# Kernel tuning notes

Hardware: AMD Instinct MI355X
Metric: run time of the kernel (lower is better)

Reference implementation:

```python
import jax, jax.numpy as jnp
import numpy as np

N = 100000
E = 1600000
D_IN = 64
D_OUT = 64
NUM_GRAPHS = 64
EPS = 1e-5


def setup_inputs() -> dict:
    key = jax.random.key(0)
    ks = jax.random.split(key, 8)
    x = jax.random.normal(ks[0], (N, D_IN), dtype=jnp.float32)
    edge_index = jax.random.randint(ks[1], (2, E), 0, N, dtype=jnp.int64)
    edge_attr = jax.random.uniform(ks[2], (E,), dtype=jnp.float32)
    batch_index = jnp.sort(jax.random.randint(ks[3], (N,), 0, NUM_GRAPHS, dtype=jnp.int64))
    s = 1.0 / np.sqrt(D_IN)
    W_rel = jax.random.uniform(ks[4], (D_OUT, D_IN), minval=-s, maxval=s, dtype=jnp.float32)
    b_rel = jax.random.uniform(ks[5], (D_OUT,), minval=-s, maxval=s, dtype=jnp.float32)
    W_root = jax.random.uniform(ks[6], (D_OUT, D_IN), minval=-s, maxval=s, dtype=jnp.float32)
    gn_weight = jnp.ones((D_OUT,), dtype=jnp.float32)
    gn_bias = jnp.zeros((D_OUT,), dtype=jnp.float32)
    gn_mean_scale = jnp.ones((D_OUT,), dtype=jnp.float32)
    return {"x": x, "edge_index": edge_index, "edge_attr": edge_attr,
            "batch_index": batch_index, "W_rel": W_rel, "b_rel": b_rel,
            "W_root": W_root, "gn_weight": gn_weight, "gn_bias": gn_bias,
            "gn_mean_scale": gn_mean_scale}


def reference(x, edge_index, edge_attr, batch_index, W_rel, b_rel, W_root,
              gn_weight, gn_bias, gn_mean_scale):
    src, dst = edge_index[0], edge_index[1]
    # GraphConv: out = W_rel @ sum_{j in N(i)} e_ij * x_j + W_root @ x_i + b
    msg = edge_attr[:, None] * x[src]                      # [E, D_IN]
    agg = jax.ops.segment_sum(msg, dst, num_segments=N)    # [N, D_IN]
    h = agg @ W_rel.T + b_rel + x @ W_root.T               # [N, D_OUT]
    h = jax.nn.relu(h)
    # GraphNorm over per-graph segments
    cnt = jax.ops.segment_sum(jnp.ones((N, 1), h.dtype), batch_index,
                              num_segments=NUM_GRAPHS)      # [G, 1]
    mean = jax.ops.segment_sum(h, batch_index, num_segments=NUM_GRAPHS) / cnt
    out = h - mean[batch_index] * gn_mean_scale
    var = jax.ops.segment_sum(out * out, batch_index, num_segments=NUM_GRAPHS) / cnt
    std = jnp.sqrt(var + EPS)[batch_index]
    return gn_weight * out / std + gn_bias
```

## Files before the change

kernel.cpp:

```cpp
#include <hip/hip_runtime.h>

#define N_NODES 100000
#define N_EDGES 1600000
#define D 64
#define NUM_GRAPHS 64
#define EPS 1e-5f

#define BSHIFT 9
#define NPB 512
#define NBUCKETS ((N_NODES + NPB - 1) / NPB)
#define BCAP 12288
#define A_THREADS 1024
#define A_EPT 8
#define A_CHUNK (A_THREADS * A_EPT)
#define NBLK_A ((N_EDGES + A_CHUNK - 1) / A_CHUNK)
#define XB ((N_NODES * 64 / 8 + 255) / 256)

#define SCAN_T 256
#define SCAN_E 8
#define SCAN_CHUNK (SCAN_T * SCAN_E)
#define NSCAN ((N_NODES + SCAN_CHUNK - 1) / SCAN_CHUNK)

typedef float f32x4 __attribute__((ext_vector_type(4)));
typedef short bf16x8 __attribute__((ext_vector_type(8)));

__device__ __forceinline__ ushort f32_to_bf16_rne(float v) {
    unsigned int bits = __float_as_uint(v);
    return (ushort)((bits + 0x7FFFu + ((bits >> 16) & 1u)) >> 16);
}

__global__ __launch_bounds__(256) void xcast_init_kernel(
    const float* __restrict__ x, ushort* __restrict__ xh,
    int* __restrict__ bucket_cur, float* __restrict__ gsum,
    float* __restrict__ gsum2, float* __restrict__ gcnt)
{
    if (blockIdx.x < XB) {
        int i = blockIdx.x * blockDim.x + threadIdx.x;
        if (i >= N_NODES * 64 / 8) return;
        const float4* src = reinterpret_cast<const float4*>(x) + (size_t)i * 2;
        float4 v0 = src[0], v1 = src[1];
        float vf[8] = {v0.x, v0.y, v0.z, v0.w, v1.x, v1.y, v1.z, v1.w};
        union { ushort us[8]; uint4 u4; } o;
        #pragma unroll
        for (int j = 0; j < 8; ++j) o.us[j] = f32_to_bf16_rne(vf[j]);
        reinterpret_cast<uint4*>(xh)[i] = o.u4;
    } else {
        int i = (blockIdx.x - XB) * 256 + threadIdx.x;
        if (i < 256) bucket_cur[i] = i * BCAP;
        if (i < NUM_GRAPHS * 64) { gsum[i] = 0.f; gsum2[i] = 0.f; }
        if (i < 64) gcnt[i] = 0.f;
    }
}

__global__ __launch_bounds__(A_THREADS) void binA_kernel(
    const int* __restrict__ src_idx, const int* __restrict__ dst_idx,
    const float* __restrict__ ea, int* __restrict__ bucket_cursor,
    unsigned long long* __restrict__ binned)
{
    __shared__ int hist[NBUCKETS];
    __shared__ int lbase[NBUCKETS];
    int tid = threadIdx.x;
    if (tid < NBUCKETS) hist[tid] = 0;
    __syncthreads();

    int base = blockIdx.x * A_CHUNK;
    int srcv[A_EPT], dstv[A_EPT];
    float wv[A_EPT];
    #pragma unroll
    for (int i = 0; i < A_EPT; ++i) {
        int e = base + i * A_THREADS + tid;
        if (e < N_EDGES) {
            srcv[i] = src_idx[e];
            dstv[i] = dst_idx[e];
            wv[i]   = ea[e];
            atomicAdd(&hist[dstv[i] >> BSHIFT], 1);
        } else {
            dstv[i] = -1; srcv[i] = 0; wv[i] = 0.f;
        }
    }
    __syncthreads();
    if (tid < NBUCKETS) lbase[tid] = atomicAdd(&bucket_cursor[tid], hist[tid]);
    __syncthreads();
    if (tid < NBUCKETS) hist[tid] = 0;
    __syncthreads();
    #pragma unroll
    for (int i = 0; i < A_EPT; ++i) {
        if (dstv[i] >= 0) {
            int b = dstv[i] >> BSHIFT;
            int r = atomicAdd(&hist[b], 1);
            unsigned int lo = (unsigned int)(srcv[i] | ((dstv[i] & (NPB - 1)) << 17));
            unsigned long long pv = (unsigned long long)lo |
                ((unsigned long long)__float_as_uint(wv[i]) << 32);
            binned[lbase[b] + r] = pv;
        }
    }
}

__global__ __launch_bounds__(256) void binB_kernel(
    const unsigned long long* __restrict__ binned,
    const int* __restrict__ bucket_cur,
    int2* __restrict__ offsets2, unsigned int* __restrict__ csr)
{
    __shared__ int dcnt[NPB];
    __shared__ int doff[NPB];
    __shared__ int psum[256];
    int tid = threadIdx.x;
    int b = blockIdx.x;
    int beg = b * BCAP;
    int n = bucket_cur[b] - beg;

    for (int i = tid; i < NPB; i += 256) dcnt[i] = 0;
    __syncthreads();
    for (int j = tid; j < n; j += 256) {
        unsigned long long pv = binned[beg + j];
        atomicAdd(&dcnt[((unsigned int)pv) >> 17], 1);
    }
    __syncthreads();
    int e0 = dcnt[2 * tid], e1 = dcnt[2 * tid + 1];
    psum[tid] = e0 + e1;
    __syncthreads();
    for (int off = 1; off < 256; off <<= 1) {
        int v = psum[tid];
        int a = (tid >= off) ? psum[tid - off] : 0;
        __syncthreads();
        psum[tid] = v + a;
        __syncthreads();
    }
    int ex = (tid == 0) ? 0 : psum[tid - 1];
    doff[2 * tid] = ex;
    doff[2 * tid + 1] = ex + e0;
    __syncthreads();
    for (int i = tid; i < NPB; i += 256) {
        int node = (b << BSHIFT) + i;
        if (node < N_NODES) {
            int s = beg + doff[i];
            int e = beg + ((i + 1 < NPB) ? doff[i + 1] : n);
            offsets2[node] = make_int2(s, e);
        }
        dcnt[i] = doff[i];
    }
    __syncthreads();
    for (int j = tid; j < n; j += 256) {
        unsigned long long pv = binned[beg + j];
        unsigned int lo = (unsigned int)pv;
        unsigned int wbits = (unsigned int)(pv >> 32);
        int dlo = lo >> 17;
        int r = atomicAdd(&dcnt[dlo], 1);
        unsigned int field = ((wbits + 0x7FFFu + ((wbits >> 16) & 1u)) >> 16) & 0x7FFFu;
        csr[beg + r] = (lo & 0x1FFFFu) | (field << 17);
    }
}

__global__ __launch_bounds__(256) void gatherh_kernel(
    const ushort* __restrict__ xh, const int2* __restrict__ offsets2,
    const unsigned int* __restrict__ csr, ushort* __restrict__ agg)
{
    int wid = (int)((blockIdx.x * blockDim.x + threadIdx.x) >> 6);
    if (wid >= N_NODES) return;
    int lane = threadIdx.x & 63;
    int2 o2 = offsets2[wid];
    int beg = __builtin_amdgcn_readfirstlane(o2.x);
    int end = __builtin_amdgcn_readfirstlane(o2.y);
    float acc[8];
    #pragma unroll
    for (int u = 0; u < 8; ++u) acc[u] = 0.f;
    int j = beg;
    for (; j + 7 < end; j += 8) {
        unsigned int e[8];
        #pragma unroll
        for (int u = 0; u < 8; ++u) e[u] = csr[j + u];
        float xv[8];
        #pragma unroll
        for (int u = 0; u < 8; ++u)
            xv[u] = __uint_as_float((unsigned int)xh[(size_t)(e[u] & 0x1FFFFu) * 64 + lane] << 16);
        #pragma unroll
        for (int u = 0; u < 8; ++u)
            acc[u] = fmaf(__uint_as_float((e[u] >> 17) << 16), xv[u], acc[u]);
    }
    for (; j < end; ++j) {
        unsigned int e0 = csr[j];
        float xv = __uint_as_float((unsigned int)xh[(size_t)(e0 & 0x1FFFFu) * 64 + lane] << 16);
        acc[0] = fmaf(__uint_as_float((e0 >> 17) << 16), xv, acc[0]);
    }
    float a = ((acc[0] + acc[1]) + (acc[2] + acc[3])) +
              ((acc[4] + acc[5]) + (acc[6] + acc[7]));
    agg[(size_t)wid * 64 + lane] = f32_to_bf16_rne(a);
}

#define DB 128
__global__ __launch_bounds__(256) void dense_mfma16_kernel(
    const ushort* __restrict__ agg, const ushort* __restrict__ xh,
    ushort* __restrict__ hout,
    const float* __restrict__ W_rel, const float* __restrict__ b_rel,
    const float* __restrict__ W_root)
{
    __shared__ unsigned int Bf[4][4][64][4];
    int tid = threadIdx.x;

    #pragma unroll
    for (int g = 0; g < 8; ++g) {
        int q = tid * 8 + g;
        int i4   = (q & 1) * 4;
        int lane = (q >> 1) & 63;
        int dt   = (q >> 7) & 3;
        int kt   = (q >> 9) & 3;
        int d = dt * 16 + (lane & 15);
        int k = kt * 32 + (lane >> 4) * 8 + i4;
        const float* Wsrc = (k < 64) ? (W_rel + d * 64 + k)
                                     : (W_root + d * 64 + (k - 64));
        float4 w = *reinterpret_cast<const float4*>(Wsrc);
        unsigned int b0 = f32_to_bf16_rne(w.x);
        unsigned int b1 = f32_to_bf16_rne(w.y);
        unsigned int b2 = f32_to_bf16_rne(w.z);
        unsigned int b3 = f32_to_bf16_rne(w.w);
        int u = i4 >> 1;
        Bf[kt][dt][lane][u]     = b0 | (b1 << 16);
        Bf[kt][dt][lane][u + 1] = b2 | (b3 << 16);
    }
    __syncthreads();

    int wid = tid >> 6, lane = tid & 63;
    int nbase = blockIdx.x * DB + wid * 32;
    int r = lane & 15;
    int k0 = (lane >> 4) * 8;

    f32x4 acc[2][4];
    #pragma unroll
    for (int nt = 0; nt < 2; ++nt)
        #pragma unroll
        for (int dt = 0; dt < 4; ++dt)
            acc[nt][dt] = (f32x4){0.f, 0.f, 0.f, 0.f};

    bf16x8 zf;
    #pragma unroll
    for (int i = 0; i < 8; ++i) zf[i] = 0;

    #pragma unroll 1
    for (int kt = 0; kt < 4; ++kt) {
        bf16x8 bh[4];
        #pragma unroll
        for (int dt = 0; dt < 4; ++dt)
            bh[dt] = *reinterpret_cast<const bf16x8*>(&Bf[kt][dt][lane][0]);
        int kk = kt * 32 + k0;
        #pragma unroll
        for (int nt = 0; nt < 2; ++nt) {
            int node = nbase + nt * 16 + r;
            bool ok = (node < N_NODES);
            const ushort* srcrow = (kk < 64)
                ? (agg + (size_t)node * 64 + kk)
                : (xh + (size_t)node * 64 + (kk - 64));
            bf16x8 a = ok ? *reinterpret_cast<const bf16x8*>(srcrow) : zf;
            #pragma unroll
            for (int dt = 0; dt < 4; ++dt)
                acc[nt][dt] = __builtin_amdgcn_mfma_f32_16x16x32_bf16(a, bh[dt], acc[nt][dt], 0, 0, 0);
        }
    }

    int rowg = (lane >> 4) * 4;
    #pragma unroll
    for (int dt = 0; dt < 4; ++dt) {
        int d = dt * 16 + r;
        float bias = b_rel[d];
        #pragma unroll
        for (int nt = 0; nt < 2; ++nt) {
            #pragma unroll
            for (int reg = 0; reg < 4; ++reg) {
                int node = nbase + nt * 16 + rowg + reg;
                if (node < N_NODES) {
                    float v = fmaxf(acc[nt][dt][reg] + bias, 0.f);
                    hout[(size_t)node * 64 + d] = f32_to_bf16_rne(v);
                }
            }
        }
    }
}

#define NPW 32
__global__ __launch_bounds__(256) void stats16_kernel(
    const ushort* __restrict__ h,
    const int* __restrict__ batch,
    float* __restrict__ gsum,
    float* __restrict__ gsum2,
    float* __restrict__ gcnt)
{
    int wave = (int)((blockIdx.x * blockDim.x + threadIdx.x) >> 6);
    int lane = threadIdx.x & 63;
    int base = wave * NPW;
    if (base >= N_NODES) return;
    int end = min(base + NPW, N_NODES);

    int gcur = batch[base];
    float s = 0.f, s2 = 0.f, cnt = 0.f;
    for (int n = base; n < end; ++n) {
        int g = batch[n];
        if (g != gcur) {
            atomicAdd(&gsum[gcur * 64 + lane], s);
            atomicAdd(&gsum2[gcur * 64 + lane], s2);
            if (lane == 0) atomicAdd(&gcnt[gcur], cnt);
            s = 0.f; s2 = 0.f; cnt = 0.f;
            gcur = g;
        }
        float v = __uint_as_float((unsigned int)h[(size_t)n * 64 + lane] << 16);
        s += v;
        s2 = fmaf(v, v, s2);
        cnt += 1.f;
    }
    atomicAdd(&gsum[gcur * 64 + lane], s);
    atomicAdd(&gsum2[gcur * 64 + lane], s2);
    if (lane == 0) atomicAdd(&gcnt[gcur], cnt);
}

__global__ __launch_bounds__(256) void finalize_kernel(
    const float* __restrict__ gsum,
    const float* __restrict__ gsum2,
    const float* __restrict__ gcnt,
    const float* __restrict__ gn_w,
    const float* __restrict__ gn_b,
    const float* __restrict__ gn_ms,
    float* __restrict__ Ag,
    float* __restrict__ Bg)
{
    int i = blockIdx.x * blockDim.x + threadIdx.x;
    if (i >= NUM_GRAPHS * 64) return;
    int g = i >> 6, d = i & 63;
    float c = fmaxf(gcnt[g], 1.f);
    float m = gsum[i] / c;
    float q = gsum2[i] / c;
    float s = gn_ms[d];
    float var = q - (2.f * s - s * s) * m * m;
    float inv = rsqrtf(fmaxf(var, 0.f) + EPS);
    float A = gn_w[d] * inv;
    Ag[i] = A;
    Bg[i] = gn_b[d] - A * s * m;
}

__global__ __launch_bounds__(256) void apply16_kernel(
    const ushort* __restrict__ h,
    const int* __restrict__ batch,
    const float* __restrict__ Ag,
    const float* __restrict__ Bg,
    float* __restrict__ out)
{
    int i = blockIdx.x * blockDim.x + threadIdx.x;
    if (i >= N_NODES * 8) return;
    int n = i >> 3;
    int q = i & 7;
    int g = batch[n];
    union { uint4 u4; ushort us[8]; } hv;
    hv.u4 = *reinterpret_cast<const uint4*>(h + (size_t)n * 64 + q * 8);
    const float4* Av = reinterpret_cast<const float4*>(Ag + g * 64 + q * 8);
    const float4* Bv = reinterpret_cast<const float4*>(Bg + g * 64 + q * 8);
    float4 A0 = Av[0], A1 = Av[1];
    float4 B0 = Bv[0], B1 = Bv[1];
    float Af[8] = {A0.x, A0.y, A0.z, A0.w, A1.x, A1.y, A1.z, A1.w};
    float Bf_[8] = {B0.x, B0.y, B0.z, B0.w, B1.x, B1.y, B1.z, B1.w};
    float4 o0, o1;
    float of[8];
    #pragma unroll
    for (int j = 0; j < 8; ++j) {
        float v = __uint_as_float((unsigned int)hv.us[j] << 16);
        of[j] = fmaf(Af[j], v, Bf_[j]);
    }
    o0.x = of[0]; o0.y = of[1]; o0.z = of[2]; o0.w = of[3];
    o1.x = of[4]; o1.y = of[5]; o1.z = of[6]; o1.w = of[7];
    float4* op = reinterpret_cast<float4*>(out + (size_t)n * 64 + q * 8);
    op[0] = o0;
    op[1] = o1;
}

__global__ __launch_bounds__(256) void hist_kernel(
    const int* __restrict__ dst_idx, int* __restrict__ deg)
{
    int e = blockIdx.x * blockDim.x + threadIdx.x;
    if (e >= N_EDGES) return;
    atomicAdd(&deg[dst_idx[e]], 1);
}

__global__ __launch_bounds__(SCAN_T) void scan1_kernel(
    const int* __restrict__ deg, int* __restrict__ offsets,
    int* __restrict__ blocksum)
{
    __shared__ int lds[SCAN_T];
    int b = blockIdx.x, t = threadIdx.x;
    int base = b * SCAN_CHUNK + t * SCAN_E;
    int v[SCAN_E];
    int s = 0;
    #pragma unroll
    for (int i = 0; i < SCAN_E; ++i) {
        v[i] = (base + i < N_NODES) ? deg[base + i] : 0;
        s += v[i];
    }
    lds[t] = s;
    __syncthreads();
    for (int off = 1; off < SCAN_T; off <<= 1) {
        int val = lds[t];
        int add = (t >= off) ? lds[t - off] : 0;
        __syncthreads();
        lds[t] = val + add;
        __syncthreads();
    }
    if (t == SCAN_T - 1) blocksum[b] = lds[SCAN_T - 1];
    int run = (t == 0) ? 0 : lds[t - 1];
    #pragma unroll
    for (int i = 0; i < SCAN_E; ++i) {
        if (base + i < N_NODES) offsets[base + i] = run;
        run += v[i];
    }
}

__global__ __launch_bounds__(64) void scan2_kernel(
    const int* __restrict__ blocksum, int* __restrict__ blockoff)
{
    __shared__ int lds[64];
    int t = threadIdx.x;
    lds[t] = (t < NSCAN) ? blocksum[t] : 0;
    __syncthreads();
    for (int off = 1; off < 64; off <<= 1) {
        int val = lds[t];
        int add = (t >= off) ? lds[t - off] : 0;
        __syncthreads();
        lds[t] = val + add;
        __syncthreads();
    }
    if (t < NSCAN) blockoff[t] = (t == 0) ? 0 : lds[t - 1];
}

__global__ __launch_bounds__(256) void scan3_kernel(
    int* __restrict__ offsets, const int* __restrict__ blockoff,
    int* __restrict__ cursor)
{
    int i = blockIdx.x * blockDim.x + threadIdx.x;
    if (i < N_NODES) {
        int v = offsets[i] + blockoff[i / SCAN_CHUNK];
        offsets[i] = v;
        cursor[i] = v;
    }
    if (i == 0) offsets[N_NODES] = N_EDGES;
}

__global__ __launch_bounds__(256) void fill_kernel(
    const int* __restrict__ src_idx, const int* __restrict__ dst_idx,
    const float* __restrict__ ea, int* __restrict__ cursor,
    int2* __restrict__ csr)
{
    int e = blockIdx.x * blockDim.x + threadIdx.x;
    if (e >= N_EDGES) return;
    int s = src_idx[e];
    int d = dst_idx[e];
    float w = ea[e];
    int pos = atomicAdd(&cursor[d], 1);
    csr[pos] = make_int2(s, __float_as_int(w));
}

__global__ __launch_bounds__(256) void gather_kernel(
    const float* __restrict__ x, const int* __restrict__ offsets,
    const int2* __restrict__ csr, float* __restrict__ agg)
{
    int wid = (int)((blockIdx.x * blockDim.x + threadIdx.x) >> 6);
    if (wid >= N_NODES) return;
    int lane = threadIdx.x & 63;
    int beg = __builtin_amdgcn_readfirstlane(offsets[wid]);
    int end = __builtin_amdgcn_readfirstlane(offsets[wid + 1]);
    float acc0 = 0.f, acc1 = 0.f;
    int j = beg;
    for (; j + 1 < end; j += 2) {
        int2 a = csr[j];
        int2 b = csr[j + 1];
        acc0 = fmaf(__int_as_float(a.y), x[(size_t)a.x * 64 + lane], acc0);
        acc1 = fmaf(__int_as_float(b.y), x[(size_t)b.x * 64 + lane], acc1);
    }
    if (j < end) {
        int2 a = csr[j];
        acc0 = fmaf(__int_as_float(a.y), x[(size_t)a.x * 64 + lane], acc0);
    }
    agg[(size_t)wid * 64 + lane] = acc0 + acc1;
}

__global__ __launch_bounds__(256) void scatter_kernel(
    const float* __restrict__ x,
    const int* __restrict__ src_idx,
    const int* __restrict__ dst_idx,
    const float* __restrict__ ea,
    float* __restrict__ agg)
{
    long long gid = (long long)blockIdx.x * blockDim.x + threadIdx.x;
    if (gid >= (long long)N_EDGES * 16) return;
    int e = (int)(gid >> 4);
    int q = (int)(gid & 15);
    int s = src_idx[e];
    int d = dst_idx[e];
    float w = ea[e];
    float4 v = reinterpret_cast<const float4*>(x)[(size_t)s * 16 + q];
    float* out = agg + (size_t)d * 64 + q * 4;
    atomicAdd(out + 0, w * v.x);
    atomicAdd(out + 1, w * v.y);
    atomicAdd(out + 2, w * v.z);
    atomicAdd(out + 3, w * v.w);
}

__global__ __launch_bounds__(256) void dense_mfma_kernel(
    float* __restrict__ aggh,
    const float* __restrict__ x,
    const float* __restrict__ W_rel,
    const float* __restrict__ b_rel,
    const float* __restrict__ W_root)
{
    __shared__ unsigned int Bf[2][4][4][64][4];
    int tid = threadIdx.x;
    #pragma unroll
    for (int g = 0; g < 8; ++g) {
        int q = tid * 8 + g;
        int i4   = (q & 1) * 4;
        int lane = (q >> 1) & 63;
        int dt   = (q >> 7) & 3;
        int kt   = (q >> 9) & 3;
        int d = dt * 16 + (lane & 15);
        int k = kt * 32 + (lane >> 4) * 8 + i4;
        const float* Wsrc = (k < 64) ? (W_rel + d * 64 + k)
                                     : (W_root + d * 64 + (k - 64));
        float4 w = *reinterpret_cast<const float4*>(Wsrc);
        float wf[4] = {w.x, w.y, w.z, w.w};
        unsigned int hi[4], lo[4];
        #pragma unroll
        for (int j = 0; j < 4; ++j) {
            unsigned int bits = __float_as_uint(wf[j]);
            hi[j] = bits >> 16;
            float resid = wf[j] - __uint_as_float(bits & 0xFFFF0000u);
            lo[j] = __float_as_uint(resid) >> 16;
        }
        int u = i4 >> 1;
        Bf[0][kt][dt][lane][u]     = hi[0] | (hi[1] << 16);
        Bf[0][kt][dt][lane][u + 1] = hi[2] | (hi[3] << 16);
        Bf[1][kt][dt][lane][u]     = lo[0] | (lo[1] << 16);
        Bf[1][kt][dt][lane][u + 1] = lo[2] | (lo[3] << 16);
    }
    __syncthreads();

    int wid = tid >> 6, lane = tid & 63;
    int nbase = blockIdx.x * DB + wid * 32;
    int r = lane & 15;
    int k0 = (lane >> 4) * 8;

    f32x4 acc[2][4];
    #pragma unroll
    for (int nt = 0; nt < 2; ++nt)
        #pragma unroll
        for (int dt = 0; dt < 4; ++dt)
            acc[nt][dt] = (f32x4){0.f, 0.f, 0.f, 0.f};

    #pragma unroll 1
    for (int kt = 0; kt < 4; ++kt) {
        bf16x8 bh[4], bl[4];
        #pragma unroll
        for (int dt = 0; dt < 4; ++dt) {
            bh[dt] = *reinterpret_cast<const bf16x8*>(&Bf[0][kt][dt][lane][0]);
            bl[dt] = *reinterpret_cast<const bf16x8*>(&Bf[1][kt][dt][lane][0]);
        }
        int kk = kt * 32 + k0;
        #pragma unroll
        for (int nt = 0; nt < 2; ++nt) {
            int node = nbase + nt * 16 + r;
            float av[8];
            if (node < N_NODES) {
                const float* srcrow = (kk < 64)
                    ? (aggh + (size_t)node * 64 + kk)
                    : (x + (size_t)node * 64 + (kk - 64));
                float4 v0 = reinterpret_cast<const float4*>(srcrow)[0];
                float4 v1 = reinterpret_cast<const float4*>(srcrow)[1];
                av[0] = v0.x; av[1] = v0.y; av[2] = v0.z; av[3] = v0.w;
                av[4] = v1.x; av[5] = v1.y; av[6] = v1.z; av[7] = v1.w;
            } else {
                #pragma unroll
                for (int i = 0; i < 8; ++i) av[i] = 0.f;
            }
            bf16x8 ah, al;
            #pragma unroll
            for (int i = 0; i < 8; ++i) {
                unsigned int bits = __float_as_uint(av[i]);
                ah[i] = (short)(bits >> 16);
                float resid = av[i] - __uint_as_float(bits & 0xFFFF0000u);
                al[i] = (short)(__float_as_uint(resid) >> 16);
            }
            #pragma unroll
            for (int dt = 0; dt < 4; ++dt) {
                acc[nt][dt] = __builtin_amdgcn_mfma_f32_16x16x32_bf16(ah, bh[dt], acc[nt][dt], 0, 0, 0);
                acc[nt][dt] = __builtin_amdgcn_mfma_f32_16x16x32_bf16(al, bh[dt], acc[nt][dt], 0, 0, 0);
                acc[nt][dt] = __builtin_amdgcn_mfma_f32_16x16x32_bf16(ah, bl[dt], acc[nt][dt], 0, 0, 0);
            }
        }
    }

    int rowg = (lane >> 4) * 4;
    #pragma unroll
    for (int dt = 0; dt < 4; ++dt) {
        int d = dt * 16 + r;
        float bias = b_rel[d];
        #pragma unroll
        for (int nt = 0; nt < 2; ++nt) {
            #pragma unroll
            for (int reg = 0; reg < 4; ++reg) {
                int node = nbase + nt * 16 + rowg + reg;
                if (node < N_NODES) {
                    float v = fmaxf(acc[nt][dt][reg] + bias, 0.f);
                    aggh[(size_t)node * 64 + d] = v;
                }
            }
        }
    }
}

#define NPW2 32
__global__ __launch_bounds__(256) void stats_kernel(
    const float* __restrict__ h,
    const int* __restrict__ batch,
    float* __restrict__ gsum,
    float* __restrict__ gsum2,
    float* __restrict__ gcnt)
{
    int wave = (int)((blockIdx.x * blockDim.x + threadIdx.x) >> 6);
    int lane = threadIdx.x & 63;
    int base = wave * NPW2;
    if (base >= N_NODES) return;
    int end = min(base + NPW2, N_NODES);

    int gcur = batch[base];
    float s = 0.f, s2 = 0.f, cnt = 0.f;
    for (int n = base; n < end; ++n) {
        int g = batch[n];
        if (g != gcur) {
            atomicAdd(&gsum[gcur * 64 + lane], s);
            atomicAdd(&gsum2[gcur * 64 + lane], s2);
            if (lane == 0) atomicAdd(&gcnt[gcur], cnt);
            s = 0.f; s2 = 0.f; cnt = 0.f;
            gcur = g;
        }
        float v = h[(size_t)n * 64 + lane];
        s += v;
        s2 = fmaf(v, v, s2);
        cnt += 1.f;
    }
    atomicAdd(&gsum[gcur * 64 + lane], s);
    atomicAdd(&gsum2[gcur * 64 + lane], s2);
    if (lane == 0) atomicAdd(&gcnt[gcur], cnt);
}

__global__ __launch_bounds__(256) void apply_kernel(
    const float* __restrict__ h,
    const int* __restrict__ batch,
    const float* __restrict__ Ag,
    const float* __restrict__ Bg,
    float* __restrict__ out)
{
    long long gid = (long long)blockIdx.x * blockDim.x + threadIdx.x;
    if (gid >= (long long)N_NODES * 16) return;
    int n = (int)(gid >> 4);
    int q = (int)(gid & 15);
    int g = batch[n];
    float4 hv = reinterpret_cast<const float4*>(h)[gid];
    float4 A = reinterpret_cast<const float4*>(Ag)[g * 16 + q];
    float4 B = reinterpret_cast<const float4*>(Bg)[g * 16 + q];
    float4 o;
    o.x = fmaf(A.x, hv.x, B.x);
    o.y = fmaf(A.y, hv.y, B.y);
    o.z = fmaf(A.z, hv.z, B.z);
    o.w = fmaf(A.w, hv.w, B.w);
    reinterpret_cast<float4*>(out)[gid] = o;
}

extern "C" void kernel_launch(void* const* d_in, const int* in_sizes, int n_in,
                              void* d_out, int out_size, void* d_ws, size_t ws_size,
                              hipStream_t stream)
{
    const float* x      = (const float*)d_in[0];
    const int*   ei     = (const int*)d_in[1];
    const float* ea     = (const float*)d_in[2];
    const int*   batch  = (const int*)d_in[3];
    const float* W_rel  = (const float*)d_in[4];
    const float* b_rel  = (const float*)d_in[5];
    const float* W_root = (const float*)d_in[6];
    const float* gn_w   = (const float*)d_in[7];
    const float* gn_b   = (const float*)d_in[8];
    const float* gn_ms  = (const float*)d_in[9];
    const int* src_idx = ei;
    const int* dst_idx = ei + N_EDGES;

    char* wsp = (char*)d_ws;

    int*   bucket_cur  = (int*)wsp;
    float* gsumN       = (float*)(bucket_cur + 256);
    float* gsum2N      = gsumN + NUM_GRAPHS * 64;
    float* gcntN       = gsum2N + NUM_GRAPHS * 64;
    int2*  offsets2    = (int2*)(gcntN + 64);
    size_t regA_off    = (((size_t)((char*)(offsets2 + N_NODES) - wsp)) + 15) & ~(size_t)15;
    size_t binned_sz   = (size_t)NBUCKETS * BCAP * 8;
    size_t hbuf_sz     = (size_t)N_NODES * 64 * 2;
    size_t regA_sz     = (binned_sz > hbuf_sz ? binned_sz : hbuf_sz);
    unsigned long long* binned = (unsigned long long*)(wsp + regA_off);
    ushort* hbuf16     = (ushort*)(wsp + regA_off);
    unsigned int* csrN = (unsigned int*)(wsp + regA_off + regA_sz);
    ushort* aggN       = (ushort*)((char*)csrN + (size_t)NBUCKETS * BCAP * 4);
    float*  AgN        = (float*)(aggN + (size_t)N_NODES * 64);
    float*  BgN        = AgN + NUM_GRAPHS * 64;
    ushort* xh         = (ushort*)(BgN + NUM_GRAPHS * 64);
    size_t reqN        = (size_t)((char*)(xh + (size_t)N_NODES * 64) - wsp);

    int*   degL     = (int*)wsp;
    float* gsumL    = (float*)(degL + N_NODES);
    float* gsum2L   = gsumL + NUM_GRAPHS * 64;
    float* gcntL    = gsum2L + NUM_GRAPHS * 64;
    size_t zeroL    = ((size_t)N_NODES + 2 * NUM_GRAPHS * 64 + 64) * 4;
    int*   offsetsL = (int*)(gcntL + 64);
    int*   blocksum = offsetsL + N_NODES + 1;
    int*   blockoff = blocksum + 64;
    int*   cursorL  = blockoff + 64;
    size_t csrL_off = (((size_t)((char*)(cursorL + N_NODES) - wsp)) + 15) & ~(size_t)15;
    int2*  csrL     = (int2*)(wsp + csrL_off);
    float* aggL     = (float*)(csrL + N_EDGES);
    float* AgL      = aggL + (size_t)N_NODES * 64;
    float* BgL      = AgL + NUM_GRAPHS * 64;
    size_t reqL     = (size_t)((char*)(BgL + NUM_GRAPHS * 64) - wsp);

    if (ws_size >= reqN) {
        xcast_init_kernel<<<XB + 16, 256, 0, stream>>>(
            x, xh, bucket_cur, gsumN, gsum2N, gcntN);
        binA_kernel<<<NBLK_A, A_THREADS, 0, stream>>>(src_idx, dst_idx, ea, bucket_cur, binned);
        binB_kernel<<<NBUCKETS, 256, 0, stream>>>(binned, bucket_cur, offsets2, csrN);
        gatherh_kernel<<<(N_NODES + 3) / 4, 256, 0, stream>>>(xh, offsets2, csrN, aggN);
        dense_mfma16_kernel<<<(N_NODES + DB - 1) / DB, 256, 0, stream>>>(
            aggN, xh, hbuf16, W_rel, b_rel, W_root);
        {
            int waves = (N_NODES + NPW - 1) / NPW;
            stats16_kernel<<<(waves + 3) / 4, 256, 0, stream>>>(hbuf16, batch, gsumN, gsum2N, gcntN);
        }
        finalize_kernel<<<(NUM_GRAPHS * 64 + 255) / 256, 256, 0, stream>>>(
            gsumN, gsum2N, gcntN, gn_w, gn_b, gn_ms, AgN, BgN);
        apply16_kernel<<<(N_NODES * 8 + 255) / 256, 256, 0, stream>>>(
            hbuf16, batch, AgN, BgN, (float*)d_out);
    } else if (ws_size >= reqL) {
        hipMemsetAsync(d_ws, 0, zeroL, stream);
        hist_kernel<<<(N_EDGES + 255) / 256, 256, 0, stream>>>(dst_idx, degL);
        scan1_kernel<<<NSCAN, SCAN_T, 0, stream>>>(degL, offsetsL, blocksum);
        scan2_kernel<<<1, 64, 0, stream>>>(blocksum, blockoff);
        scan3_kernel<<<(N_NODES + 255) / 256, 256, 0, stream>>>(offsetsL, blockoff, cursorL);
        fill_kernel<<<(N_EDGES + 255) / 256, 256, 0, stream>>>(src_idx, dst_idx, ea, cursorL, csrL);
        gather_kernel<<<(N_NODES + 3) / 4, 256, 0, stream>>>(x, offsetsL, csrL, aggL);
        dense_mfma_kernel<<<(N_NODES + DB - 1) / DB, 256, 0, stream>>>(
            aggL, x, W_rel, b_rel, W_root);
        {
            int waves = (N_NODES + NPW2 - 1) / NPW2;
            stats_kernel<<<(waves + 3) / 4, 256, 0, stream>>>(aggL, batch, gsumL, gsum2L, gcntL);
        }
        finalize_kernel<<<(NUM_GRAPHS * 64 + 255) / 256, 256, 0, stream>>>(
            gsumL, gsum2L, gcntL, gn_w, gn_b, gn_ms, AgL, BgL);
        {
            long long total = (long long)N_NODES * 16;
            apply_kernel<<<(int)((total + 255) / 256), 256, 0, stream>>>(
                aggL, batch, AgL, BgL, (float*)d_out);
        }
    } else {
        float* agg = (float*)(gcntL + 64);
        float* Ag  = agg + (size_t)N_NODES * 64;
        float* Bg  = Ag + NUM_GRAPHS * 64;
        size_t zb = zeroL + (size_t)N_NODES * 64 * 4;
        hipMemsetAsync(d_ws, 0, zb, stream);
        long long total = (long long)N_EDGES * 16;
        scatter_kernel<<<(int)((total + 255) / 256), 256, 0, stream>>>(
            x, src_idx, dst_idx, ea, agg);
        dense_mfma_kernel<<<(N_NODES + DB - 1) / DB, 256, 0, stream>>>(
            agg, x, W_rel, b_rel, W_root);
        {
            int waves = (N_NODES + NPW2 - 1) / NPW2;
            stats_kernel<<<(waves + 3) / 4, 256, 0, stream>>>(agg, batch, gsumL, gsum2L, gcntL);
        }
        finalize_kernel<<<(NUM_GRAPHS * 64 + 255) / 256, 256, 0, stream>>>(
            gsumL, gsum2L, gcntL, gn_w, gn_b, gn_ms, Ag, Bg);
        {
            long long t2 = (long long)N_NODES * 16;
            apply_kernel<<<(int)((t2 + 255) / 256), 256, 0, stream>>>(
                agg, batch, Ag, Bg, (float*)d_out);
        }
    }
}
```

Measured before the change: 152.7 us.

## Gather four nodes per wave with 16 lanes each using 8-byte loads

The bf16 neighbor gather now gives each node 16 lanes instead of a whole 64-lane wave, so one wave covers four destination nodes. Each lane loads four bf16 features as a uint2 and keeps four accumulators per edge, unrolled over two edges. The aim is fewer, wider memory requests and more nodes in flight per wave. In exchange, degree imbalance between the four nodes in a wave causes divergence, edge-level ILP drops from eight edges to two, and the edge bounds are no longer wave-uniform.

```diff
diff --git a/kernel.cpp b/kernel.cpp
--- a/kernel.cpp
+++ b/kernel.cpp
@@ -28,6 +28,12 @@
     unsigned int bits = __float_as_uint(v);
     return (ushort)((bits + 0x7FFFu + ((bits >> 16) & 1u)) >> 16);
 }
+__device__ __forceinline__ float bf16lo_to_f32(unsigned int u) {
+    return __uint_as_float(u << 16);
+}
+__device__ __forceinline__ float bf16hi_to_f32(unsigned int u) {
+    return __uint_as_float(u & 0xFFFF0000u);
+}
 
 __global__ __launch_bounds__(256) void xcast_init_kernel(
     const float* __restrict__ x, ushort* __restrict__ xh,
@@ -151,40 +157,57 @@
     }
 }
 
-__global__ __launch_bounds__(256) void gatherh_kernel(
+__global__ __launch_bounds__(256) void gatherh4_kernel(
     const ushort* __restrict__ xh, const int2* __restrict__ offsets2,
     const unsigned int* __restrict__ csr, ushort* __restrict__ agg)
 {
-    int wid = (int)((blockIdx.x * blockDim.x + threadIdx.x) >> 6);
-    if (wid >= N_NODES) return;
-    int lane = threadIdx.x & 63;
-    int2 o2 = offsets2[wid];
-    int beg = __builtin_amdgcn_readfirstlane(o2.x);
-    int end = __builtin_amdgcn_readfirstlane(o2.y);
-    float acc[8];
-    #pragma unroll
-    for (int u = 0; u < 8; ++u) acc[u] = 0.f;
+    int tid = threadIdx.x;
+    int wave = tid >> 6, lane = tid & 63;
+    int grp = lane >> 4, sl = lane & 15;
+    int node = blockIdx.x * 16 + wave * 4 + grp;
+    bool ok = (node < N_NODES);
+    int2 o2 = ok ? offsets2[node] : make_int2(0, 0);
+    int beg = o2.x, end = o2.y;
+
+    float a0 = 0.f, a1 = 0.f, a2 = 0.f, a3 = 0.f;
+    float b0 = 0.f, b1 = 0.f, b2 = 0.f, b3 = 0.f;
     int j = beg;
-    for (; j + 7 < end; j += 8) {
-        unsigned int e[8];
-        #pragma unroll
-        for (int u = 0; u < 8; ++u) e[u] = csr[j + u];
-        float xv[8];
-        #pragma unroll
-        for (int u = 0; u < 8; ++u)
-            xv[u] = __uint_as_float((unsigned int)xh[(size_t)(e[u] & 0x1FFFFu) * 64 + lane] << 16);
-        #pragma unroll
-        for (int u = 0; u < 8; ++u)
-            acc[u] = fmaf(__uint_as_float((e[u] >> 17) << 16), xv[u], acc[u]);
-    }
-    for (; j < end; ++j) {
+    for (; j + 1 < end; j += 2) {
         unsigned int e0 = csr[j];
-        float xv = __uint_as_float((unsigned int)xh[(size_t)(e0 & 0x1FFFFu) * 64 + lane] << 16);
-        acc[0] = fmaf(__uint_as_float((e0 >> 17) << 16), xv, acc[0]);
-    }
-    float a = ((acc[0] + acc[1]) + (acc[2] + acc[3])) +
-              ((acc[4] + acc[5]) + (acc[6] + acc[7]));
-    agg[(size_t)wid * 64 + lane] = f32_to_bf16_rne(a);
+        unsigned int e1 = csr[j + 1];
+        uint2 x0 = *reinterpret_cast<const uint2*>(
+            xh + (size_t)(e0 & 0x1FFFFu) * 64 + sl * 4);
+        uint2 x1 = *reinterpret_cast<const uint2*>(
+            xh + (size_t)(e1 & 0x1FFFFu) * 64 + sl * 4);
+        float w0 = __uint_as_float((e0 >> 17) << 16);
+        float w1 = __uint_as_float((e1 >> 17) << 16);
+        a0 = fmaf(w0, bf16lo_to_f32(x0.x & 0xFFFFu), a0);
+        a1 = fmaf(w0, bf16hi_to_f32(x0.x), a1);
+        a2 = fmaf(w0, bf16lo_to_f32(x0.y & 0xFFFFu), a2);
+        a3 = fmaf(w0, bf16hi_to_f32(x0.y), a3);
+        b0 = fmaf(w1, bf16lo_to_f32(x1.x & 0xFFFFu), b0);
+        b1 = fmaf(w1, bf16hi_to_f32(x1.x), b1);
+        b2 = fmaf(w1, bf16lo_to_f32(x1.y & 0xFFFFu), b2);
+        b3 = fmaf(w1, bf16hi_to_f32(x1.y), b3);
+    }
+    if (j < end) {
+        unsigned int e0 = csr[j];
+        uint2 x0 = *reinterpret_cast<const uint2*>(
+            xh + (size_t)(e0 & 0x1FFFFu) * 64 + sl * 4);
+        float w0 = __uint_as_float((e0 >> 17) << 16);
+        a0 = fmaf(w0, bf16lo_to_f32(x0.x & 0xFFFFu), a0);
+        a1 = fmaf(w0, bf16hi_to_f32(x0.x), a1);
+        a2 = fmaf(w0, bf16lo_to_f32(x0.y & 0xFFFFu), a2);
+        a3 = fmaf(w0, bf16hi_to_f32(x0.y), a3);
+    }
+    if (ok) {
+        unsigned int lo = (unsigned int)f32_to_bf16_rne(a0 + b0)
+                        | ((unsigned int)f32_to_bf16_rne(a1 + b1) << 16);
+        unsigned int hi = (unsigned int)f32_to_bf16_rne(a2 + b2)
+                        | ((unsigned int)f32_to_bf16_rne(a3 + b3) << 16);
+        *reinterpret_cast<uint2*>(agg + (size_t)node * 64 + sl * 4) =
+            make_uint2(lo, hi);
+    }
 }
 
 #define DB 128
@@ -725,7 +748,7 @@
             x, xh, bucket_cur, gsumN, gsum2N, gcntN);
         binA_kernel<<<NBLK_A, A_THREADS, 0, stream>>>(src_idx, dst_idx, ea, bucket_cur, binned);
         binB_kernel<<<NBUCKETS, 256, 0, stream>>>(binned, bucket_cur, offsets2, csrN);
-        gatherh_kernel<<<(N_NODES + 3) / 4, 256, 0, stream>>>(xh, offsets2, csrN, aggN);
+        gatherh4_kernel<<<(N_NODES + 15) / 16, 256, 0, stream>>>(xh, offsets2, csrN, aggN);
         dense_mfma16_kernel<<<(N_NODES + DB - 1) / DB, 256, 0, stream>>>(
             aggN, xh, hbuf16, W_rel, b_rel, W_root);
         {
```

After: 145.0 us. -5.1%, faster.
